# Kernel optimization log

Measured on AMD Instinct MI355X. Metric: run time of the kernel, lower is better.

Reference implementation:

```python
import jax, jax.numpy as jnp
import numpy as np
from jax import lax

D = 30   # embedding_dim (hardcoded in repo)
Q = 30   # question length
N = 4000 # number of sentences in doc
S = 100  # tokens per sentence
K = 5    # k_for_maxpool
SLOPE = 0.1  # LeakyReLU negative slope


def setup_inputs() -> dict:
    key = jax.random.key(0)
    ks = jax.random.split(key, 20)
    rn = lambda k, sh: jax.random.normal(k, sh, dtype=jnp.float32)
    ru = lambda k, sh: jax.random.uniform(k, sh, dtype=jnp.float32)
    return {
        "doc_sents_embeds": rn(ks[0], (N, S, D)),
        "sents_gaf": ru(ks[1], (N, 3)),
        "question_embeds": rn(ks[2], (Q, D)),
        "q_idfs": ru(ks[3], (Q, 1)),
        "doc_gaf": ru(ks[4], (4,)),
        "conv1_w": rn(ks[5], (D, D, 3)) * 0.1,
        "conv1_b": rn(ks[6], (D,)) * 0.1,
        "conv2_w": rn(ks[7], (D, D, 3)) * 0.1,
        "conv2_b": rn(ks[8], (D,)) * 0.1,
        "qw_W": rn(ks[9], (1, D + 1)) * 0.1,
        "qw_b": rn(ks[10], (1,)) * 0.1,
        "lq1_W": rn(ks[11], (8, 6)) * 0.1,
        "lq1_b": rn(ks[12], (8,)) * 0.1,
        "lq2_W": rn(ks[13], (1, 8)) * 0.1,
        "lq2_b": rn(ks[14], (1,)) * 0.1,
        "so_W": rn(ks[15], (1, 4)) * 0.1,
        "so_b": rn(ks[16], (1,)) * 0.1,
        "fl_W": rn(ks[17], (1, 5)) * 0.1,
        "fl_b": rn(ks[18], (1,)) * 0.1,
    }


def _leaky(x):
    return jnp.where(x >= 0, x, SLOPE * x)


def _conv_block(x, w, b):
    # x: [B, L, D]. torch Conv1d(D, D, 3, padding=2) then slice [1:L+1]
    # is exactly a 'same' conv with padding 1 on each side; then residual add.
    y = lax.conv_general_dilated(x.transpose(0, 2, 1), w, (1,), [(1, 1)],
                                 dimension_numbers=("NCH", "OIH", "NCH"))
    y = _leaky(y + b[None, :, None])
    return y.transpose(0, 2, 1) + x


def _cos_sim(A, B):
    # A: [Q, D], B: [N, S, D] -> [N, Q, S] (num/den as in torch my_cosine_sim)
    num = jnp.einsum("qd,nsd->nqs", A, B)
    den = jnp.linalg.norm(A, axis=-1)[None, :, None] * jnp.linalg.norm(B, axis=-1)[:, None, :]
    return num / den


def _pool(sim):
    # sort-based k-max pooling -> [max, avg_of_top_k]; sim: [N, Q, S] -> [N, Q, 2]
    vals = lax.top_k(sim, K)[0]  # descending
    return jnp.stack([vals[..., 0], vals.mean(-1)], axis=-1)


def reference(doc_sents_embeds, sents_gaf, question_embeds, q_idfs, doc_gaf,
              conv1_w, conv1_b, conv2_w, conv2_b, qw_W, qw_b,
              lq1_W, lq1_b, lq2_W, lq2_b, so_W, so_b, fl_W, fl_b):
    # question context (two residual trigram convs)
    q_conv = _conv_block(question_embeds[None], conv1_w, conv1_b)
    q_conv = _conv_block(q_conv, conv2_w, conv2_b)[0]          # [Q, D]
    # question term weights
    qw_in = jnp.concatenate([q_conv, q_idfs], axis=-1)          # [Q, D+1]
    q_weights = jax.nn.softmax((qw_in @ qw_W.T + qw_b)[:, 0])   # [Q]
    # sentence context convs (batched over all sentences)
    conv_res = _conv_block(doc_sents_embeds, conv1_w, conv1_b)
    conv_res = _conv_block(conv_res, conv2_w, conv2_b)          # [N, S, D]
    # similarity matrices
    sim_insens = _cos_sim(question_embeds, doc_sents_embeds)    # [N, Q, S]
    sim_oh = (sim_insens > 1.0 - 1e-3).astype(sim_insens.dtype)
    sim_sens = _cos_sim(q_conv, conv_res)
    # k-max pooling and per-q tiny MLP attention
    feats = jnp.concatenate([_pool(sim_oh), _pool(sim_insens), _pool(sim_sens)], axis=-1)  # [N, Q, 6]
    lo = _leaky(feats @ lq1_W.T + lq1_b) @ lq2_W.T + lq2_b      # [N, Q, 1]
    lo = lo[..., 0] * q_weights[None, :]
    sent_emit = lo.sum(-1) / Q                                  # [N]
    # per-sentence output layer
    sent_feats = jnp.concatenate([sents_gaf, sent_emit[:, None]], axis=-1)  # [N, 4]
    sent_scores = jax.nn.sigmoid((sent_feats @ so_W.T + so_b)[:, 0])        # [N]
    # doc-level score
    doc_rep = jnp.concatenate([jnp.max(sent_scores)[None], doc_gaf])        # [5]
    final = doc_rep @ fl_W.T + fl_b                                          # [1]
    return final, sent_scores
```

## Files before the change

kernel.cpp:

```cpp
#include <hip/hip_runtime.h>
#include <hip/hip_bf16.h>

#define SLOPE 0.1f

#define OFF_QW    1816
#define OFF_QNI   1846
#define OFF_QNS   1876
#define OFF_QNN   1906
#define OFF_B1    4606
#define OFF_B2    7336
#define OFF_LQ1W  7366
#define OFF_LQ1B  7414
#define OFF_LQ2W  7422
#define OFF_LQ2B  7430
#define OFF_SOW   7431
#define OFF_SOB   7435
#define OFF_FLW   7436
#define OFF_FLB   7441
#define U16_QEA   16384
#define U16_QCA   17408
#define U16_WB1   18432
#define U16_WB2   21504

#define XDW 1620

typedef __attribute__((ext_vector_type(8))) __bf16 bf16x8;
typedef __attribute__((ext_vector_type(4))) float f32x4;

union Frag { uint4 u4; uint u[4]; bf16x8 v; };

__device__ __forceinline__ float bf2f(ushort h) {
    union { uint u; float f; } c; c.u = ((uint)h) << 16; return c.f;
}
__device__ __forceinline__ ushort f2bf(float f) {
    union { float f; uint u; } c; c.f = f;
    uint u = c.u;
    return (ushort)((u + 0x7FFFu + ((u >> 16) & 1u)) >> 16);
}
__device__ __forceinline__ float ldx(const void* p, long i, int bf) {
    if (bf) return bf2f(((const ushort*)p)[i]);
    return ((const float*)p)[i];
}
__device__ __forceinline__ uint pk2(float lo, float hi) {
    uint r;
    asm("v_cvt_pk_bf16_f32 %0, %1, %2" : "=v"(r) : "v"(lo), "v"(hi));
    return r;
}
__device__ __forceinline__ float blo(uint u) { return __uint_as_float(u << 16); }
__device__ __forceinline__ float bhi(uint u) { return __uint_as_float(u & 0xFFFF0000u); }
__device__ __forceinline__ float lk(float x) { return fmaxf(x, SLOPE * x); }

#define CE(x, y) { float _hi = fmaxf(x, y), _lo = fminf(x, y); x = _hi; y = _lo; }

__device__ __forceinline__ void sort4d(float& a, float& b, float& c, float& d) {
    CE(a, b); CE(c, d); CE(a, c); CE(b, d); CE(b, c);
}
__device__ __forceinline__ void merge44_5(const float* a, const float* b, float* t) {
    t[0] = fmaxf(a[0], b[0]);
    t[1] = fmaxf(fminf(a[0], b[0]), fmaxf(a[1], b[1]));
    t[2] = fmaxf(fmaxf(fminf(a[0], b[1]), fminf(a[1], b[0])), fmaxf(a[2], b[2]));
    t[3] = fmaxf(fmaxf(fminf(a[0], b[2]), fminf(a[1], b[1])),
                 fmaxf(fminf(a[2], b[0]), fmaxf(a[3], b[3])));
    t[4] = fmaxf(fmaxf(fminf(a[0], b[3]), fminf(a[1], b[2])),
                 fmaxf(fminf(a[2], b[1]), fminf(a[3], b[0])));
}
__device__ __forceinline__ void merge54_5(const float* a, const float* b, float* t) {
    t[0] = fmaxf(a[0], b[0]);
    t[1] = fmaxf(fminf(a[0], b[0]), fmaxf(a[1], b[1]));
    t[2] = fmaxf(fmaxf(fminf(a[0], b[1]), fminf(a[1], b[0])), fmaxf(a[2], b[2]));
    t[3] = fmaxf(fmaxf(fminf(a[0], b[2]), fminf(a[1], b[1])),
                 fmaxf(fminf(a[2], b[0]), fmaxf(a[3], b[3])));
    t[4] = fmaxf(fmaxf(fmaxf(fminf(a[0], b[3]), fminf(a[1], b[2])),
                       fmaxf(fminf(a[2], b[1]), fminf(a[3], b[0]))), a[4]);
}
__device__ __forceinline__ void merge55_5(const float* a, const float* b, float* t) {
    t[0] = fmaxf(a[0], b[0]);
    t[1] = fmaxf(fminf(a[0], b[0]), fmaxf(a[1], b[1]));
    t[2] = fmaxf(fmaxf(fminf(a[0], b[1]), fminf(a[1], b[0])), fmaxf(a[2], b[2]));
    t[3] = fmaxf(fmaxf(fminf(a[0], b[2]), fminf(a[1], b[1])),
                 fmaxf(fminf(a[2], b[0]), fmaxf(a[3], b[3])));
    t[4] = fmaxf(fmaxf(fmaxf(fminf(a[0], b[3]), fminf(a[1], b[2])),
                       fmaxf(fminf(a[2], b[1]), fminf(a[3], b[0]))),
                 fmaxf(a[4], b[4]));
}

__device__ __forceinline__ int detect_bf(const void* doc_in, int tid, int* scnt) {
    if (tid == 0) *scnt = 0;
    __syncthreads();
    const ushort* p = (const ushort*)doc_in;
    int local = 0;
    for (int i = tid; i < 4096; i += 256) {
        unsigned e = (p[i] >> 7) & 0xFFu;
        if (e != 0u && (e < 100u || e > 134u)) local++;
    }
    atomicAdd(scnt, local);
    __syncthreads();
    return (*scnt > 200) ? 0 : 1;
}

__global__ __launch_bounds__(256) void k_prep(
        const void* doc_in,
        const void* qe_in, const void* qidf_in,
        const void* w1_in, const void* b1_in,
        const void* w2_in, const void* b2_in,
        const void* qwW_in, const void* qwb_in,
        const void* lq1W_in, const void* lq1b_in,
        const void* lq2W_in, const void* lq2b_in,
        const void* soW_in, const void* sob_in,
        const void* flW_in, const void* flb_in,
        float* ws) {
    const int tid = threadIdx.x;
    const int blk = blockIdx.x;
    __shared__ float QE[900], T1[900], QC[900], W[2700], IDF[32], LG[32];
    __shared__ int scnt;

    const int bf = detect_bf(doc_in, tid, &scnt);
    ushort* wsu = (ushort*)ws;

    if (blk == 1) {
        if (tid == 0) { ((int*)ws)[0] = bf; }
        if (tid < 30) ws[OFF_B1 + tid] = ldx(b1_in, tid, bf);
        if (tid < 48) ws[OFF_LQ1W + tid] = ldx(lq1W_in, tid, bf);
        if (tid < 8)  { ws[OFF_LQ1B + tid] = ldx(lq1b_in, tid, bf);
                        ws[OFF_LQ2W + tid] = ldx(lq2W_in, tid, bf); }
        if (tid < 4)  ws[OFF_SOW + tid] = ldx(soW_in, tid, bf);
        if (tid < 5)  ws[OFF_FLW + tid] = ldx(flW_in, tid, bf);
        if (tid == 1) { ws[OFF_LQ2B] = ldx(lq2b_in, 0, bf);
                        ws[OFF_SOB]  = ldx(sob_in, 0, bf);
                        ws[OFF_FLB]  = ldx(flb_in, 0, bf); }
        for (int i = tid; i < 3072; i += 256) {
            int o = i / 96, kk = i % 96;
            int k = kk >> 5, ii = kk & 31;
            float v1 = 0.f;
            if (o < 30 && ii < 30) v1 = ldx(w1_in, (long)o*90 + ii*3 + k, bf);
            wsu[U16_WB1 + i] = f2bf(v1);
        }
        return;
    }
    if (blk == 2) {
        if (tid < 30) ws[OFF_B2 + tid] = ldx(b2_in, tid, bf);
        for (int i = tid; i < 3072; i += 256) {
            int o = i / 96, kk = i % 96;
            int k = kk >> 5, ii = kk & 31;
            float v2 = 0.f;
            if (o < 30 && ii < 30) v2 = ldx(w2_in, (long)o*90 + ii*3 + k, bf);
            wsu[U16_WB2 + i] = f2bf(v2);
        }
        return;
    }

    if (tid == 0) { ((int*)ws)[0] = bf; }

    for (int i = tid; i < 900; i += 256) QE[i] = ldx(qe_in, i, bf);
    if (tid < 30) IDF[tid] = ldx(qidf_in, tid, bf);
    for (int i = tid; i < 2700; i += 256) W[i] = ldx(w1_in, i, bf);
    __syncthreads();

    for (int idx = tid; idx < 900; idx += 256) {
        int s = idx / 30, o = idx % 30;
        float acc = ldx(b1_in, o, bf);
        for (int k = 0; k < 3; ++k) {
            int t = s + k - 1;
            if (t < 0 || t >= 30) continue;
            for (int i = 0; i < 30; ++i) acc += QE[t*30 + i] * W[o*90 + i*3 + k];
        }
        acc = acc >= 0.f ? acc : SLOPE * acc;
        T1[idx] = acc + QE[idx];
    }
    __syncthreads();
    for (int i = tid; i < 2700; i += 256) W[i] = ldx(w2_in, i, bf);
    __syncthreads();
    for (int idx = tid; idx < 900; idx += 256) {
        int s = idx / 30, o = idx % 30;
        float acc = ldx(b2_in, o, bf);
        for (int k = 0; k < 3; ++k) {
            int t = s + k - 1;
            if (t < 0 || t >= 30) continue;
            for (int i = 0; i < 30; ++i) acc += T1[t*30 + i] * W[o*90 + i*3 + k];
        }
        acc = acc >= 0.f ? acc : SLOPE * acc;
        QC[idx] = acc + T1[idx];
    }
    __syncthreads();

    if (tid < 30) {
        float s1 = 0.f, s2 = 0.f;
        for (int d = 0; d < 30; ++d) {
            float a = QE[tid*30 + d]; s1 += a*a;
            float b = QC[tid*30 + d]; s2 += b*b;
        }
        float n1 = sqrtf(s1);
        ws[OFF_QNN + tid] = n1;
        ws[OFF_QNI + tid] = 1.0f / n1;
        ws[OFF_QNS + tid] = 1.0f / sqrtf(s2);
        float z = ldx(qwb_in, 0, bf);
        for (int d = 0; d < 30; ++d) z += QC[tid*30 + d] * ldx(qwW_in, d, bf);
        z += IDF[tid] * ldx(qwW_in, 30, bf);
        LG[tid] = z;
    }
    __syncthreads();
    if (tid == 0) {
        float m = -1e30f;
        for (int q = 0; q < 30; ++q) m = fmaxf(m, LG[q]);
        float sum = 0.f, e[30];
        for (int q = 0; q < 30; ++q) { e[q] = expf(LG[q] - m); sum += e[q]; }
        for (int q = 0; q < 30; ++q) ws[OFF_QW + q] = e[q] / sum;
    }
    for (int i = tid; i < 1024; i += 256) {
        int q = i >> 5, d = i & 31;
        float ve = (q < 30 && d < 30) ? QE[q*30 + d] : 0.f;
        float vc = (q < 30 && d < 30) ? QC[q*30 + d] : 0.f;
        wsu[U16_QEA + i] = f2bf(ve);
        wsu[U16_QCA + i] = f2bf(vc);
    }
}

__global__ __launch_bounds__(128, 5) void k_main(const void* doc_in, const void* gaf_in,
                                                 void* out, float* ws) {
    const int n = blockIdx.x;
    const int tid = threadIdx.x;
    const int bf = ((const int*)ws)[0];
    const int lane = tid & 63;
    const int wid = tid >> 6;
    const int l15 = lane & 15;
    const int quad = lane >> 4;

    __shared__ __align__(16) uint X[XDW];
    __shared__ __align__(16) float INVX[112];
    __shared__ float FE[30][6];

    const ushort* wsu = (const ushort*)ws;
    const uint4* qeA = (const uint4*)(wsu + U16_QEA);
    const uint4* qcA = (const uint4*)(wsu + U16_QCA);
    const uint4* wb1 = (const uint4*)(wsu + U16_WB1);
    const uint4* wb2 = (const uint4*)(wsu + U16_WB2);

    float ga0 = ldx(gaf_in, (long)n*3 + 0, bf);
    float ga1 = ldx(gaf_in, (long)n*3 + 1, bf);
    float ga2 = ldx(gaf_in, (long)n*3 + 2, bf);

    if (tid < 60) {
        int j = (tid < 15) ? tid : ((tid < 45) ? (1500 + tid) : (1560 + tid));
        X[j] = 0u;
    }
    if (tid >= 100 && tid < 112) INVX[tid] = 0.f;
    if (bf) {
        const uint4* g = (const uint4*)((const ushort*)doc_in + (size_t)n * 3000);
        for (int j = tid; j < 375; j += 128) {
            uint4 v = g[j];
            int d = 15 + 4 * j;
            X[d] = v.x; X[d + 1] = v.y; X[d + 2] = v.z; X[d + 3] = v.w;
        }
    } else {
        const float4* p4 = (const float4*)((const float*)doc_in + (size_t)n * 3000);
        for (int j = tid; j < 750; j += 128) {
            float4 f = p4[j];
            int d = 15 + 2 * j;
            X[d]     = pk2(f.x, f.y);
            X[d + 1] = pk2(f.z, f.w);
        }
    }
    __syncthreads();

    if (tid < 100) {
        const uint* r = X + (tid + 1) * 15;
        float s = 0.f;
        #pragma unroll
        for (int i = 0; i < 15; ++i) {
            uint u = r[i];
            float lo = __uint_as_float(u << 16);
            float hi = __uint_as_float(u & 0xFFFF0000u);
            s += lo * lo + hi * hi;
        }
        INVX[tid] = 1.f / sqrtf(s);
    } else if (tid < 115) {
        X[103*15 + (tid - 100)] = X[48*15 + (tid - 100)];
    } else if (tid < 128 + 2) {  }
    if (tid >= 100 && tid < 115) {  }
    if (tid < 15 || true) {  }
    if (tid >= 113 && tid < 128) {
        X[104*15 + (tid - 113)] = X[49*15 + (tid - 113)];
    }
    __syncthreads();

    auto sim_pool = [&](const uint4* qa, int iqOff, int fbase, bool do_oh) {
        const int q = wid * 16 + l15;
        Frag b;
        b.u4 = qa[q * 4 + quad];
        f32x4 acc[7];
        #pragma unroll
        for (int mt = 0; mt < 7; ++mt) {
            int m = mt * 16 + l15;
            Frag a;
            if (m < 100) {
                int base = (m + 1) * 15 + quad * 4;
                a.u[0] = X[base];     a.u[1] = X[base + 1];
                a.u[2] = X[base + 2]; a.u[3] = X[base + 3];
            } else { a.u[0] = a.u[1] = a.u[2] = a.u[3] = 0u; }
            f32x4 z = {0.f, 0.f, 0.f, 0.f};
            acc[mt] = __builtin_amdgcn_mfma_f32_16x16x32_bf16(a.v, b.v, z, 0, 0, 0);
        }
        const float4* INVX4 = (const float4*)INVX;
        float thr = (do_oh && q < 30) ? 0.999f * ws[OFF_QNN + q] : 1e30f;
        float iq  = (q < 30) ? ws[iqOff + q] : 0.f;
        float g[7][4];
        int cnt = 0;
        #pragma unroll
        for (int mt = 0; mt < 7; ++mt) {
            float4 ix = INVX4[mt * 4 + quad];
            float ixa[4] = {ix.x, ix.y, ix.z, ix.w};
            #pragma unroll
            for (int r = 0; r < 4; ++r) {
                float u = acc[mt][r] * ixa[r];
                if (mt == 6 && (quad * 4 + r) >= 4) u = -1e30f;
                g[mt][r] = u;
                if (do_oh) cnt += (u > thr) ? 1 : 0;
            }
        }
        #pragma unroll
        for (int mt = 0; mt < 7; ++mt) sort4d(g[mt][0], g[mt][1], g[mt][2], g[mt][3]);
        float p0[5], p1[5], p2[5], q0[5], q1[5], t[5];
        merge44_5(g[0], g[1], p0);
        merge44_5(g[2], g[3], p1);
        merge44_5(g[4], g[5], p2);
        merge55_5(p0, p1, q0);
        merge54_5(p2, g[6], q1);
        merge55_5(q0, q1, t);
        #pragma unroll
        for (int d = 16; d < 64; d <<= 1) {
            float pp[5];
            pp[0] = __shfl_xor(t[0], d); pp[1] = __shfl_xor(t[1], d);
            pp[2] = __shfl_xor(t[2], d); pp[3] = __shfl_xor(t[3], d);
            pp[4] = __shfl_xor(t[4], d);
            if (do_oh) cnt += __shfl_xor(cnt, d);
            float tn[5];
            merge55_5(t, pp, tn);
            t[0] = tn[0]; t[1] = tn[1]; t[2] = tn[2]; t[3] = tn[3]; t[4] = tn[4];
        }
        if (quad == 0 && q < 30) {
            if (do_oh) {
                FE[q][0] = cnt > 0 ? 1.f : 0.f;
                FE[q][1] = (float)(cnt > 5 ? 5 : cnt) * 0.2f;
            }
            FE[q][fbase]     = t[0] * iq;
            FE[q][fbase + 1] = (t[0] + t[1] + t[2] + t[3] + t[4]) * 0.2f * iq;
        }
    };

    auto conv_inplace = [&](const uint4* wb, int bOff, int mirIn48, int mirIn49,
                            bool dupOut, bool donorm) {
        const int mtb = wid ? 3 : 0;
        const int mte = wid ? 6 : 2;
        Frag wf0[3], wf1[3];
        #pragma unroll
        for (int k = 0; k < 3; ++k) {
            wf0[k].u4 = wb[l15 * 12 + k * 4 + quad];
            wf1[k].u4 = wb[(16 + l15) * 12 + k * 4 + quad];
        }
        float b40[4], b41[4];
        #pragma unroll
        for (int r = 0; r < 4; ++r) {
            int o0 = quad * 4 + r, o1 = 16 + o0;
            b40[r] = ws[bOff + o0];
            b41[r] = (o1 < 30) ? ws[bOff + o1] : 0.f;
        }
        auto load_row = [&](int row) {
            int rr = row;
            if (wid == 1 && row == 48) rr = mirIn48;
            if (wid == 0 && row == 49) rr = mirIn49;
            Frag f;
            int base = rr * 15 + quad * 4;
            f.u[0] = X[base];     f.u[1] = X[base + 1];
            f.u[2] = X[base + 2]; f.u[3] = X[base + 3];
            return f;
        };
        Frag zf; zf.u[0] = zf.u[1] = zf.u[2] = zf.u[3] = 0u;
        Frag f0n = (mtb * 16 + l15 < 100) ? load_row(mtb * 16 + l15) : zf;
        for (int mt = mtb; mt <= mte; ++mt) {
            const int s = mt * 16 + l15;
            const bool sv = (s < 100);
            Frag f0 = f0n, f1 = zf, f2 = zf;
            if (sv) { f1 = load_row(s + 1); f2 = load_row(s + 2); }
            if (mt < mte) {
                int s2 = (mt + 1) * 16 + l15;
                f0n = (s2 < 100) ? load_row(s2) : zf;
            }
            const int db = (s + 1) * 15 + quad * 2;
            uint u0 = 0u, u1 = 0u, u2 = 0u, u3 = 0u;
            if (sv) {
                uint2 ua = *(const uint2*)(X + db);
                uint2 ub = *(const uint2*)(X + db + 8);
                u0 = ua.x; u1 = ua.y; u2 = ub.x; u3 = ub.y;
            }
            f32x4 a0 = {0.f, 0.f, 0.f, 0.f}, a1 = {0.f, 0.f, 0.f, 0.f};
            a0 = __builtin_amdgcn_mfma_f32_16x16x32_bf16(wf0[0].v, f0.v, a0, 0, 0, 0);
            a1 = __builtin_amdgcn_mfma_f32_16x16x32_bf16(wf1[0].v, f0.v, a1, 0, 0, 0);
            a0 = __builtin_amdgcn_mfma_f32_16x16x32_bf16(wf0[1].v, f1.v, a0, 0, 0, 0);
            a1 = __builtin_amdgcn_mfma_f32_16x16x32_bf16(wf1[1].v, f1.v, a1, 0, 0, 0);
            a0 = __builtin_amdgcn_mfma_f32_16x16x32_bf16(wf0[2].v, f2.v, a0, 0, 0, 0);
            a1 = __builtin_amdgcn_mfma_f32_16x16x32_bf16(wf1[2].v, f2.v, a1, 0, 0, 0);
            __builtin_amdgcn_sched_barrier(0);
            float ss = 0.f;
            if (sv) {
                float v0 = lk(a0[0] + b40[0]) + blo(u0);
                float v1 = lk(a0[1] + b40[1]) + bhi(u0);
                float v2 = lk(a0[2] + b40[2]) + blo(u1);
                float v3 = lk(a0[3] + b40[3]) + bhi(u1);
                uint s01 = pk2(v0, v1), s23 = pk2(v2, v3);
                *(uint2*)(X + db) = make_uint2(s01, s23);
                float w0 = lk(a1[0] + b41[0]) + blo(u2);
                float w1 = lk(a1[1] + b41[1]) + bhi(u2);
                uint s45 = pk2(w0, w1);
                ss = v0*v0 + v1*v1 + v2*v2 + v3*v3 + w0*w0 + w1*w1;
                uint s67 = 0u;
                if (quad < 3) {
                    float w2 = lk(a1[2] + b41[2]) + blo(u3);
                    float w3 = lk(a1[3] + b41[3]) + bhi(u3);
                    s67 = pk2(w2, w3);
                    *(uint2*)(X + db + 8) = make_uint2(s45, s67);
                    ss += w2*w2 + w3*w3;
                } else {
                    X[db + 8] = s45;
                }
                if (dupOut) {
                    if (wid == 0 && mt == 2 && l15 == 15) {
                        int mdb = 105*15 + quad*2;
                        *(uint2*)(X + mdb) = make_uint2(s01, s23);
                        if (quad < 3) *(uint2*)(X + mdb + 8) = make_uint2(s45, s67);
                        else          X[mdb + 8] = s45;
                    }
                    if (wid == 1 && mt == 3 && l15 == 0) {
                        int mdb = 106*15 + quad*2;
                        *(uint2*)(X + mdb) = make_uint2(s01, s23);
                        if (quad < 3) *(uint2*)(X + mdb + 8) = make_uint2(s45, s67);
                        else          X[mdb + 8] = s45;
                    }
                }
            }
            if (donorm) {
                ss += __shfl_xor(ss, 16);
                ss += __shfl_xor(ss, 32);
                if (quad == 0 && sv) INVX[s] = 1.f / sqrtf(ss);
            }
        }
    };

    sim_pool(qeA, OFF_QNI, 2, true);
    __syncthreads();

    conv_inplace(wb1, OFF_B1, 103, 104, true, false);
    __syncthreads();

    conv_inplace(wb2, OFF_B2, 105, 106, false, true);
    __syncthreads();

    sim_pool(qcA, OFF_QNS, 4, false);
    __syncthreads();

    if (wid == 0) {
        float val = 0.f;
        if (lane < 30) {
            float lo = ws[OFF_LQ2B];
            #pragma unroll
            for (int j = 0; j < 8; ++j) {
                float h = ws[OFF_LQ1B + j];
                #pragma unroll
                for (int f = 0; f < 6; ++f) h += FE[lane][f] * ws[OFF_LQ1W + j*6 + f];
                h = lk(h);
                lo += h * ws[OFF_LQ2W + j];
            }
            val = lo * ws[OFF_QW + lane];
        }
        #pragma unroll
        for (int d = 32; d >= 1; d >>= 1) val += __shfl_xor(val, d);
        if (lane == 0) {
            float emit = val * (1.f / 30.f);
            float z = ws[OFF_SOB];
            z += ga0 * ws[OFF_SOW + 0];
            z += ga1 * ws[OFF_SOW + 1];
            z += ga2 * ws[OFF_SOW + 2];
            z += emit * ws[OFF_SOW + 3];
            float sc = 1.f / (1.f + expf(-z));
            if (bf) ((__hip_bfloat16*)out)[1 + n] = __float2bfloat16(sc);
            else    ((float*)out)[1 + n] = sc;
        }
    }
}

__global__ __launch_bounds__(256) void k_final(const void* docgaf_in, void* out, const float* ws) {
    const int tid = threadIdx.x;
    const int bf = ((const int*)ws)[0];
    __shared__ float red[256];
    float m = -1e30f;
    for (int i = tid; i < 4000; i += 256) {
        float v = bf ? __bfloat162float(((const __hip_bfloat16*)out)[1 + i])
                     : ((const float*)out)[1 + i];
        m = fmaxf(m, v);
    }
    red[tid] = m;
    __syncthreads();
    for (int off = 128; off > 0; off >>= 1) {
        if (tid < off) red[tid] = fmaxf(red[tid], red[tid + off]);
        __syncthreads();
    }
    if (tid == 0) {
        float f = ws[OFF_FLB] + red[0] * ws[OFF_FLW + 0];
        for (int i = 0; i < 4; ++i) f += ldx(docgaf_in, i, bf) * ws[OFF_FLW + 1 + i];
        if (bf) ((__hip_bfloat16*)out)[0] = __float2bfloat16(f);
        else    ((float*)out)[0] = f;
    }
}

extern "C" void kernel_launch(void* const* d_in, const int* in_sizes, int n_in,
                              void* d_out, int out_size, void* d_ws, size_t ws_size,
                              hipStream_t stream) {
    float* ws = (float*)d_ws;
    k_prep<<<3, 256, 0, stream>>>(d_in[0], d_in[2], d_in[3], d_in[5], d_in[6], d_in[7], d_in[8],
                                  d_in[9], d_in[10], d_in[11], d_in[12], d_in[13], d_in[14],
                                  d_in[15], d_in[16], d_in[17], d_in[18], ws);
    k_main<<<4000, 128, 0, stream>>>(d_in[0], d_in[1], d_out, ws);
    k_final<<<1, 256, 0, stream>>>(d_in[4], d_out, ws);
}
```

Before: 174.9 us.

## Map one sentence per wavefront, drop block barriers and row mirroring

Each 256-thread block now holds four independent wavefronts, and each wavefront processes one whole sentence in its own shared-memory slice. This removes all __syncthreads, the split of conv tiles across two waves, and the mirrored halo rows that were needed for in-place convolution across waves. In exchange, each wave does twice the MFMA and pooling work serially, and each sentence loses intra-sentence parallelism. The aim is to cut barrier and halo overhead and raise occupancy with smaller per-sentence LDS.

```diff
diff --git a/kernel.cpp b/kernel.cpp
--- a/kernel.cpp
+++ b/kernel.cpp
@@ -22,7 +22,7 @@
 #define U16_WB1   18432
 #define U16_WB2   21504
 
-#define XDW 1620
+#define XDW 1548
 
 typedef __attribute__((ext_vector_type(8))) __bf16 bf16x8;
 typedef __attribute__((ext_vector_type(4))) float f32x4;
@@ -215,19 +215,23 @@
     }
 }
 
-__global__ __launch_bounds__(128, 5) void k_main(const void* doc_in, const void* gaf_in,
+__global__ __launch_bounds__(256, 4) void k_main(const void* doc_in, const void* gaf_in,
                                                  void* out, float* ws) {
-    const int n = blockIdx.x;
     const int tid = threadIdx.x;
+    const int w = tid >> 6;
+    const int lane = tid & 63;
+    const int n = blockIdx.x * 4 + w;
     const int bf = ((const int*)ws)[0];
-    const int lane = tid & 63;
-    const int wid = tid >> 6;
     const int l15 = lane & 15;
     const int quad = lane >> 4;
 
-    __shared__ __align__(16) uint X[XDW];
-    __shared__ __align__(16) float INVX[112];
-    __shared__ float FE[30][6];
+    __shared__ __align__(16) uint Xs_[4][XDW];
+    __shared__ __align__(16) float INVXs_[4][112];
+    __shared__ float FEs_[4][30][6];
+
+    uint* X = Xs_[w];
+    float* INVX = INVXs_[w];
+    float (*FE)[6] = FEs_[w];
 
     const ushort* wsu = (const ushort*)ws;
     const uint4* qeA = (const uint4*)(wsu + U16_QEA);
@@ -239,52 +243,44 @@
     float ga1 = ldx(gaf_in, (long)n*3 + 1, bf);
     float ga2 = ldx(gaf_in, (long)n*3 + 2, bf);
 
-    if (tid < 60) {
-        int j = (tid < 15) ? tid : ((tid < 45) ? (1500 + tid) : (1560 + tid));
+    if (lane < 45) {
+        int j = (lane < 15) ? lane : (1500 + lane);
         X[j] = 0u;
-    }
-    if (tid >= 100 && tid < 112) INVX[tid] = 0.f;
+    } else if (lane < 57) {
+        INVX[100 + (lane - 45)] = 0.f;
+    }
     if (bf) {
         const uint4* g = (const uint4*)((const ushort*)doc_in + (size_t)n * 3000);
-        for (int j = tid; j < 375; j += 128) {
+        for (int j = lane; j < 375; j += 64) {
             uint4 v = g[j];
             int d = 15 + 4 * j;
             X[d] = v.x; X[d + 1] = v.y; X[d + 2] = v.z; X[d + 3] = v.w;
         }
     } else {
         const float4* p4 = (const float4*)((const float*)doc_in + (size_t)n * 3000);
-        for (int j = tid; j < 750; j += 128) {
+        for (int j = lane; j < 750; j += 64) {
             float4 f = p4[j];
             int d = 15 + 2 * j;
             X[d]     = pk2(f.x, f.y);
             X[d + 1] = pk2(f.z, f.w);
         }
     }
-    __syncthreads();
-
-    if (tid < 100) {
-        const uint* r = X + (tid + 1) * 15;
+
+    for (int r = lane; r < 100; r += 64) {
+        const uint* rp = X + (r + 1) * 15;
         float s = 0.f;
         #pragma unroll
         for (int i = 0; i < 15; ++i) {
-            uint u = r[i];
+            uint u = rp[i];
             float lo = __uint_as_float(u << 16);
             float hi = __uint_as_float(u & 0xFFFF0000u);
             s += lo * lo + hi * hi;
         }
-        INVX[tid] = 1.f / sqrtf(s);
-    } else if (tid < 115) {
-        X[103*15 + (tid - 100)] = X[48*15 + (tid - 100)];
-    } else if (tid < 128 + 2) {  }
-    if (tid >= 100 && tid < 115) {  }
-    if (tid < 15 || true) {  }
-    if (tid >= 113 && tid < 128) {
-        X[104*15 + (tid - 113)] = X[49*15 + (tid - 113)];
-    }
-    __syncthreads();
-
-    auto sim_pool = [&](const uint4* qa, int iqOff, int fbase, bool do_oh) {
-        const int q = wid * 16 + l15;
+        INVX[r] = 1.f / sqrtf(s);
+    }
+
+    auto sim_pool = [&](const uint4* qa, int iqOff, int fbase, bool do_oh, int qbase) {
+        const int q = qbase + l15;
         Frag b;
         b.u4 = qa[q * 4 + quad];
         f32x4 acc[7];
@@ -347,10 +343,7 @@
         }
     };
 
-    auto conv_inplace = [&](const uint4* wb, int bOff, int mirIn48, int mirIn49,
-                            bool dupOut, bool donorm) {
-        const int mtb = wid ? 3 : 0;
-        const int mte = wid ? 6 : 2;
+    auto conv_inplace = [&](const uint4* wb, int bOff, bool donorm) {
         Frag wf0[3], wf1[3];
         #pragma unroll
         for (int k = 0; k < 3; ++k) {
@@ -365,23 +358,20 @@
             b41[r] = (o1 < 30) ? ws[bOff + o1] : 0.f;
         }
         auto load_row = [&](int row) {
-            int rr = row;
-            if (wid == 1 && row == 48) rr = mirIn48;
-            if (wid == 0 && row == 49) rr = mirIn49;
             Frag f;
-            int base = rr * 15 + quad * 4;
+            int base = row * 15 + quad * 4;
             f.u[0] = X[base];     f.u[1] = X[base + 1];
             f.u[2] = X[base + 2]; f.u[3] = X[base + 3];
             return f;
         };
         Frag zf; zf.u[0] = zf.u[1] = zf.u[2] = zf.u[3] = 0u;
-        Frag f0n = (mtb * 16 + l15 < 100) ? load_row(mtb * 16 + l15) : zf;
-        for (int mt = mtb; mt <= mte; ++mt) {
+        Frag f0n = (l15 < 100) ? load_row(l15) : zf;
+        for (int mt = 0; mt < 7; ++mt) {
             const int s = mt * 16 + l15;
             const bool sv = (s < 100);
             Frag f0 = f0n, f1 = zf, f2 = zf;
             if (sv) { f1 = load_row(s + 1); f2 = load_row(s + 2); }
-            if (mt < mte) {
+            if (mt < 6) {
                 int s2 = (mt + 1) * 16 + l15;
                 f0n = (s2 < 100) ? load_row(s2) : zf;
             }
@@ -406,36 +396,19 @@
                 float v1 = lk(a0[1] + b40[1]) + bhi(u0);
                 float v2 = lk(a0[2] + b40[2]) + blo(u1);
                 float v3 = lk(a0[3] + b40[3]) + bhi(u1);
-                uint s01 = pk2(v0, v1), s23 = pk2(v2, v3);
-                *(uint2*)(X + db) = make_uint2(s01, s23);
+                *(uint2*)(X + db) = make_uint2(pk2(v0, v1), pk2(v2, v3));
                 float w0 = lk(a1[0] + b41[0]) + blo(u2);
                 float w1 = lk(a1[1] + b41[1]) + bhi(u2);
                 uint s45 = pk2(w0, w1);
                 ss = v0*v0 + v1*v1 + v2*v2 + v3*v3 + w0*w0 + w1*w1;
-                uint s67 = 0u;
                 if (quad < 3) {
                     float w2 = lk(a1[2] + b41[2]) + blo(u3);
                     float w3 = lk(a1[3] + b41[3]) + bhi(u3);
-                    s67 = pk2(w2, w3);
-                    *(uint2*)(X + db + 8) = make_uint2(s45, s67);
+                    *(uint2*)(X + db + 8) = make_uint2(s45, pk2(w2, w3));
                     ss += w2*w2 + w3*w3;
                 } else {
                     X[db + 8] = s45;
                 }
-                if (dupOut) {
-                    if (wid == 0 && mt == 2 && l15 == 15) {
-                        int mdb = 105*15 + quad*2;
-                        *(uint2*)(X + mdb) = make_uint2(s01, s23);
-                        if (quad < 3) *(uint2*)(X + mdb + 8) = make_uint2(s45, s67);
-                        else          X[mdb + 8] = s45;
-                    }
-                    if (wid == 1 && mt == 3 && l15 == 0) {
-                        int mdb = 106*15 + quad*2;
-                        *(uint2*)(X + mdb) = make_uint2(s01, s23);
-                        if (quad < 3) *(uint2*)(X + mdb + 8) = make_uint2(s45, s67);
-                        else          X[mdb + 8] = s45;
-                    }
-                }
             }
             if (donorm) {
                 ss += __shfl_xor(ss, 16);
@@ -445,19 +418,16 @@
         }
     };
 
-    sim_pool(qeA, OFF_QNI, 2, true);
-    __syncthreads();
-
-    conv_inplace(wb1, OFF_B1, 103, 104, true, false);
-    __syncthreads();
-
-    conv_inplace(wb2, OFF_B2, 105, 106, false, true);
-    __syncthreads();
-
-    sim_pool(qcA, OFF_QNS, 4, false);
-    __syncthreads();
-
-    if (wid == 0) {
+    sim_pool(qeA, OFF_QNI, 2, true, 0);
+    sim_pool(qeA, OFF_QNI, 2, true, 16);
+
+    conv_inplace(wb1, OFF_B1, false);
+    conv_inplace(wb2, OFF_B2, true);
+
+    sim_pool(qcA, OFF_QNS, 4, false, 0);
+    sim_pool(qcA, OFF_QNS, 4, false, 16);
+
+    {
         float val = 0.f;
         if (lane < 30) {
             float lo = ws[OFF_LQ2B];
@@ -518,6 +488,6 @@
     k_prep<<<3, 256, 0, stream>>>(d_in[0], d_in[2], d_in[3], d_in[5], d_in[6], d_in[7], d_in[8],
                                   d_in[9], d_in[10], d_in[11], d_in[12], d_in[13], d_in[14],
                                   d_in[15], d_in[16], d_in[17], d_in[18], ws);
-    k_main<<<4000, 128, 0, stream>>>(d_in[0], d_in[1], d_out, ws);
+    k_main<<<1000, 256, 0, stream>>>(d_in[0], d_in[1], d_out, ws);
     k_final<<<1, 256, 0, stream>>>(d_in[4], d_out, ws);
 }
```

Measured after the change: 182.6 us. +4.4%, slower.
